# Kernel tuning notes

Hardware: AMD Instinct MI355X
Metric: run time of the kernel (lower is better)

## Reference

```python
import jax, jax.numpy as jnp
import numpy as np

HEADS = 4
TOKEN_CH = 128
D_HEAD = TOKEN_CH // HEADS  # 32


def setup_inputs() -> dict:
    key = jax.random.key(0)
    ks = jax.random.split(key, 12)
    B, QC, Z, H, W = 4, 256, 16, 32, 32
    N, KVC = 256, 512
    s = lambda k, shape, fan: jax.random.normal(k, shape, jnp.float32) * (1.0 / np.sqrt(fan))
    return {
        "feat":   jax.random.normal(ks[0], (B, QC, Z, H, W), jnp.float32),
        "tokens": jax.random.normal(ks[1], (B, N, KVC), jnp.float32),
        "qw":   s(ks[2], (TOKEN_CH, QC), QC),      # Conv3d 1x1 -> [out, in]
        "qb":   jnp.zeros((TOKEN_CH,), jnp.float32),
        "kw":   s(ks[3], (TOKEN_CH, KVC), KVC),    # Linear, no bias
        "vw":   s(ks[4], (TOKEN_CH, KVC), KVC),
        "projw": s(ks[5], (QC, TOKEN_CH), TOKEN_CH),
        "projb": jnp.zeros((QC,), jnp.float32),
        "ff1w": s(ks[6], (QC * 2, QC), QC),
        "ff1b": jnp.zeros((QC * 2,), jnp.float32),
        "ff2w": s(ks[7], (QC, QC * 2), QC * 2),
        "ff2b": jnp.zeros((QC,), jnp.float32),
        "gate": jnp.zeros((1,), jnp.float32),
    }


def _conv1x1(x, w, b):
    # x: [B, Cin, Z, H, W], w: [Cout, Cin] -> [B, Cout, Z, H, W]
    return jnp.einsum('bczhw,oc->bozhw', x, w) + b[None, :, None, None, None]


def reference(feat, tokens, qw, qb, kw, vw, projw, projb, ff1w, ff1b, ff2w, ff2b, gate):
    B, C, Z, H, W = feat.shape
    S = Z * H * W
    scale = D_HEAD ** (-0.5)

    # Q: conv1x1 then split heads -> [B, nh, S, dh]
    q = _conv1x1(feat, qw, qb).reshape(B, HEADS, D_HEAD, S).transpose(0, 1, 3, 2)
    # K, V: linear (no bias) -> [B, nh, N, dh]
    k = jnp.einsum('bnc,tc->bnt', tokens, kw).reshape(B, -1, HEADS, D_HEAD).transpose(0, 2, 1, 3)
    v = jnp.einsum('bnc,tc->bnt', tokens, vw).reshape(B, -1, HEADS, D_HEAD).transpose(0, 2, 1, 3)

    attn = jax.nn.softmax(jnp.einsum('bhsd,bhnd->bhsn', q, k) * scale, axis=-1)
    out = jnp.einsum('bhsn,bhnd->bhsd', attn, v)  # [B, nh, S, dh]

    # merge heads back to channel-first volume: b (nh dh) z h w
    out = out.transpose(0, 1, 3, 2).reshape(B, TOKEN_CH, Z, H, W)
    out = _conv1x1(out, projw, projb)

    out = feat + jnp.tanh(gate[0]) * out
    ff = _conv1x1(jax.nn.silu(_conv1x1(out, ff1w, ff1b)), ff2w, ff2b)
    return out + ff
```

## Files before the change

kernel.cpp:

```cpp
#include <hip/hip_runtime.h>

#define NB 4
#define QC 256
#define SD 16384
#define NT 256
#define KVC 512
#define TC 128
#define NH 4
#define DH 32
#define TSP 64

typedef unsigned short u16;
typedef unsigned int u32;
typedef __attribute__((ext_vector_type(8))) short bf16x8;
typedef __attribute__((ext_vector_type(4))) float f32x4;

__device__ __forceinline__ float b2f(u16 u) {
  unsigned int v = ((unsigned int)u) << 16;
  return __builtin_bit_cast(float, v);
}
__device__ __forceinline__ u16 f2b(float f) {
  unsigned int x = __builtin_bit_cast(unsigned int, f);
  unsigned int r = (x + 0x7fffu + ((x >> 16) & 1u)) >> 16;
  return (u16)r;
}
__device__ __forceinline__ u16 f2b_fast(float f) {
  return (u16)((__builtin_bit_cast(unsigned int, f) + 0x8000u) >> 16);
}
__device__ __forceinline__ u32 pk2(float a, float b) {
  u32 ua = __builtin_bit_cast(u32, a) + 0x8000u;
  u32 ub = __builtin_bit_cast(u32, b) + 0x8000u;
  return __builtin_amdgcn_perm(ub, ua, 0x07060302u);
}

__device__ __forceinline__ int swz(int row, int col) {
  return (row << 8) + (col ^ ((row & 7) << 3));
}

__global__ __launch_bounds__(256) void prep_kernel(
    const float* __restrict__ ff1w, const float* __restrict__ ff2w,
    u16* __restrict__ w1p, u16* __restrict__ w2p,
    const float* __restrict__ tokens, const float* __restrict__ kw,
    const float* __restrict__ vw, const float* __restrict__ gate,
    float* __restrict__ ws_kv) {
  int bid = blockIdx.x;
  if (bid < 128) {
    int idx = bid * 256 + threadIdx.x;
    int lane = idx & 63;
    int m = lane & 15, q = lane >> 4;
    if (idx < 16384) {
      int kblk = (idx >> 6) & 7;
      int jblk = idx >> 9;
      const float* src = ff1w + (size_t)(jblk * 16 + m) * QC + kblk * 32 + q * 8;
      u16* dst = w1p + (size_t)idx * 8;
#pragma unroll
      for (int i = 0; i < 8; i++) dst[i] = f2b(src[i]);
    } else {
      int s2 = idx - 16384;
      int kblk = (s2 >> 6) & 15;
      int oblk = s2 >> 10;
      const float* src = ff2w + (size_t)(oblk * 16 + m) * KVC + kblk * 32 + q * 8;
      u16* dst = w2p + (size_t)s2 * 8;
#pragma unroll
      for (int i = 0; i < 8; i++) dst[i] = f2b(src[i]);
    }
  }
  float tg = tanhf(gate[0]);
  if (tg == 0.0f) return;
  {
    int b = bid >> 8;
    int n = bid & 255;
    __shared__ float tok[KVC];
    for (int c = threadIdx.x; c < KVC; c += 256)
      tok[c] = tokens[((size_t)(b * NT + n)) * KVC + c];
    __syncthreads();
    int tid = threadIdx.x;
    int t = tid & 127;
    const float* w = (tid < 128) ? kw : vw;
    const float* wr = w + (size_t)t * KVC;
    float acc = 0.f;
    for (int c = 0; c < KVC; c += 4) {
      float4 wv = *(const float4*)(wr + c);
      acc += tok[c] * wv.x + tok[c + 1] * wv.y + tok[c + 2] * wv.z + tok[c + 3] * wv.w;
    }
    int h = t >> 5, d = t & 31;
    float* dst = ws_kv + ((tid < 128) ? 0 : NB * NH * NT * DH);
    dst[(((b * NH + h) * NT) + n) * DH + d] = acc;
  }
}

__global__ __launch_bounds__(512, 4) void fused_kernel(
    const float* __restrict__ feat, const float* __restrict__ qw,
    const float* __restrict__ qb, const float* __restrict__ projw,
    const float* __restrict__ projb, const float* __restrict__ ff1b,
    const float* __restrict__ ff2b, const u16* __restrict__ w1p,
    const u16* __restrict__ w2p, const float* __restrict__ gate,
    const float* __restrict__ ws_kv, float* __restrict__ out) {
  __shared__ u16 sX[64 * 256];
  __shared__ u16 sH[64 * 256];

  int b = blockIdx.x >> 8;
  int s0 = (blockIdx.x & 255) * TSP;
  int tid = threadIdx.x;
  int w = tid >> 6;
  int lane = tid & 63;
  int lm = lane & 15, lq = lane >> 4;

  {
    const float* fb = feat + (((size_t)b * QC) << 14) + s0;
    int cq = (tid >> 4) * 4;
    int sq = (tid & 15) * 4;
#pragma unroll
    for (int it = 0; it < 2; ++it) {
      int c = it * 128 + cq;
      float4 r0 = *(const float4*)(fb + ((size_t)(c + 0) << 14) + sq);
      float4 r1 = *(const float4*)(fb + ((size_t)(c + 1) << 14) + sq);
      float4 r2 = *(const float4*)(fb + ((size_t)(c + 2) << 14) + sq);
      float4 r3 = *(const float4*)(fb + ((size_t)(c + 3) << 14) + sq);
      uint2 d0, d1, d2, d3;
      d0.x = pk2(r0.x, r1.x); d0.y = pk2(r2.x, r3.x);
      d1.x = pk2(r0.y, r1.y); d1.y = pk2(r2.y, r3.y);
      d2.x = pk2(r0.z, r1.z); d2.y = pk2(r2.z, r3.z);
      d3.x = pk2(r0.w, r1.w); d3.y = pk2(r2.w, r3.w);
      *(uint2*)&sX[swz(sq + 0, c)] = d0;
      *(uint2*)&sX[swz(sq + 1, c)] = d1;
      *(uint2*)&sX[swz(sq + 2, c)] = d2;
      *(uint2*)&sX[swz(sq + 3, c)] = d3;
    }
  }
  float tg = tanhf(gate[0]);
  __syncthreads();

  if (tg != 0.0f) {
    if (w < 4) {
      float qreg[DH];
#pragma unroll
      for (int d = 0; d < DH; d++) {
        int o = w * DH + d;
        float a = qb[o];
        const float* qr = qw + (size_t)o * QC;
        for (int c = 0; c < QC; c += 4) {
          float4 wv = *(const float4*)(qr + c);
          a += b2f(sX[swz(lane, c + 0)]) * wv.x;
          a += b2f(sX[swz(lane, c + 1)]) * wv.y;
          a += b2f(sX[swz(lane, c + 2)]) * wv.z;
          a += b2f(sX[swz(lane, c + 3)]) * wv.w;
        }
        qreg[d] = a;
      }
      const float* Kp = ws_kv + (size_t)(b * NH + w) * NT * DH;
      const float* Vp = Kp + NB * NH * NT * DH;
      float m_ = -1e30f, l_ = 0.f;
      float oacc[DH];
#pragma unroll
      for (int d = 0; d < DH; d++) oacc[d] = 0.f;
      const float scale = 0.17677669529663687f;
      for (int n = 0; n < NT; n++) {
        const float* kr = Kp + n * DH;
        float s = 0.f;
#pragma unroll
        for (int d = 0; d < DH; d++) s += qreg[d] * kr[d];
        s *= scale;
        float nm = fmaxf(m_, s);
        float p = __expf(s - nm);
        float al = __expf(m_ - nm);
        const float* vr = Vp + n * DH;
        l_ = l_ * al + p;
#pragma unroll
        for (int d = 0; d < DH; d++) oacc[d] = oacc[d] * al + p * vr[d];
        m_ = nm;
      }
      float inv = 1.0f / l_;
#pragma unroll
      for (int d = 0; d < DH; d++)
        sH[swz(lane, w * DH + d)] = f2b(oacc[d] * inv);
    }
    __syncthreads();
    for (int ci = 0; ci < 32; ci++) {
      int c = w * 32 + ci;
      float a = projb[c];
      const float* pr = projw + (size_t)c * TC;
      for (int t = 0; t < TC; t += 4) {
        float4 wv = *(const float4*)(pr + t);
        a += b2f(sH[swz(lane, t + 0)]) * wv.x;
        a += b2f(sH[swz(lane, t + 1)]) * wv.y;
        a += b2f(sH[swz(lane, t + 2)]) * wv.z;
        a += b2f(sH[swz(lane, t + 3)]) * wv.w;
      }
      float o1 = b2f(sX[swz(lane, c)]) + tg * a;
      sX[swz(lane, c)] = f2b(o1);
    }
    __syncthreads();
  }

  f32x4 acc2[2][4];
#pragma unroll
  for (int t = 0; t < 2; t++) {
    float b2v = ff2b[(w * 2 + t) * 16 + lm];
    f32x4 iv = {b2v, b2v, b2v, b2v};
#pragma unroll
    for (int m = 0; m < 4; m++) acc2[t][m] = iv;
  }

#pragma unroll 1
  for (int ch = 0; ch < 2; ++ch) {
    f32x4 acc1[2][4];
#pragma unroll
    for (int t = 0; t < 2; t++) {
      float b1v = ff1b[ch * 256 + (w * 2 + t) * 16 + lm];
      f32x4 iv = {b1v, b1v, b1v, b1v};
#pragma unroll
      for (int m = 0; m < 4; m++) acc1[t][m] = iv;
    }
    {
      int jb0 = ch * 16 + w * 2;
      const u16* p0 = w1p + (((size_t)jb0 * 8) * 64 + lane) * 8;
      const u16* p1 = p0 + 4096;
      bf16x8 c0 = *(const bf16x8*)(p0);
      bf16x8 c1 = *(const bf16x8*)(p1);
      bf16x8 n0 = *(const bf16x8*)(p0 + 512);
      bf16x8 n1 = *(const bf16x8*)(p1 + 512);
#pragma unroll
      for (int k = 0; k < 8; ++k) {
        bf16x8 f0, f1;
        if (k < 6) {
          f0 = *(const bf16x8*)(p0 + (size_t)(k + 2) * 512);
          f1 = *(const bf16x8*)(p1 + (size_t)(k + 2) * 512);
        }
        int col = k * 32 + lq * 8;
#pragma unroll
        for (int m = 0; m < 4; m++) {
          bf16x8 a = *(const bf16x8*)&sX[swz(m * 16 + lm, col)];
          acc1[0][m] = __builtin_amdgcn_mfma_f32_16x16x32_bf16(a, c0, acc1[0][m], 0, 0, 0);
          acc1[1][m] = __builtin_amdgcn_mfma_f32_16x16x32_bf16(a, c1, acc1[1][m], 0, 0, 0);
        }
        c0 = n0; c1 = n1;
        if (k < 6) { n0 = f0; n1 = f1; }
      }
    }
    __syncthreads();
#pragma unroll
    for (int t = 0; t < 2; t++) {
      int jl = (w * 2 + t) * 16 + lm;
#pragma unroll
      for (int m = 0; m < 4; m++) {
        int sb = m * 16 + lq * 4;
        f32x4 v = acc1[t][m];
#pragma unroll
        for (int r = 0; r < 4; r++) {
          float x = v[r];
          float sl = x * __builtin_amdgcn_rcpf(1.f + __expf(-x));
          sH[swz(sb + r, jl)] = f2b_fast(sl);
        }
      }
    }
    const u16* qp0 = w2p + (((size_t)((w * 2) * 16 + ch * 8)) * 64 + lane) * 8;
    const u16* qp1 = qp0 + 8192;
    bf16x8 d0 = *(const bf16x8*)(qp0);
    bf16x8 d1 = *(const bf16x8*)(qp1);
    bf16x8 e0 = *(const bf16x8*)(qp0 + 512);
    bf16x8 e1 = *(const bf16x8*)(qp1 + 512);
    __syncthreads();
#pragma unroll
    for (int k = 0; k < 8; ++k) {
      bf16x8 f0, f1;
      if (k < 6) {
        f0 = *(const bf16x8*)(qp0 + (size_t)(k + 2) * 512);
        f1 = *(const bf16x8*)(qp1 + (size_t)(k + 2) * 512);
      }
      int col = k * 32 + lq * 8;
#pragma unroll
      for (int m = 0; m < 4; m++) {
        bf16x8 a = *(const bf16x8*)&sH[swz(m * 16 + lm, col)];
        acc2[0][m] = __builtin_amdgcn_mfma_f32_16x16x32_bf16(a, d0, acc2[0][m], 0, 0, 0);
        acc2[1][m] = __builtin_amdgcn_mfma_f32_16x16x32_bf16(a, d1, acc2[1][m], 0, 0, 0);
      }
      d0 = e0; d1 = e1;
      if (k < 6) { e0 = f0; e1 = f1; }
    }
  }

#pragma unroll
  for (int t = 0; t < 2; t++) {
    int c = (w * 2 + t) * 16 + lm;
#pragma unroll
    for (int m = 0; m < 4; m++) {
      int sb = m * 16 + lq * 4;
      f32x4 v = acc2[t][m];
      float4 ov;
      ov.x = v[0] + b2f(sX[swz(sb + 0, c)]);
      ov.y = v[1] + b2f(sX[swz(sb + 1, c)]);
      ov.z = v[2] + b2f(sX[swz(sb + 2, c)]);
      ov.w = v[3] + b2f(sX[swz(sb + 3, c)]);
      *(float4*)(out + (((size_t)(b * QC + c)) << 14) + s0 + sb) = ov;
    }
  }
}

extern "C" void kernel_launch(void* const* d_in, const int* in_sizes, int n_in,
                              void* d_out, int out_size, void* d_ws, size_t ws_size,
                              hipStream_t stream) {
  const float* feat   = (const float*)d_in[0];
  const float* tokens = (const float*)d_in[1];
  const float* qw     = (const float*)d_in[2];
  const float* qb     = (const float*)d_in[3];
  const float* kw     = (const float*)d_in[4];
  const float* vw     = (const float*)d_in[5];
  const float* projw  = (const float*)d_in[6];
  const float* projb  = (const float*)d_in[7];
  const float* ff1w   = (const float*)d_in[8];
  const float* ff1b   = (const float*)d_in[9];
  const float* ff2w   = (const float*)d_in[10];
  const float* ff2b   = (const float*)d_in[11];
  const float* gate   = (const float*)d_in[12];
  float* out = (float*)d_out;

  u16* w1p = (u16*)d_ws;
  u16* w2p = w1p + 131072;
  float* ws_kv = (float*)((char*)d_ws + 524288);

  prep_kernel<<<dim3(NB * NT), dim3(256), 0, stream>>>(
      ff1w, ff2w, w1p, w2p, tokens, kw, vw, gate, ws_kv);
  fused_kernel<<<dim3(NB * (SD / TSP)), dim3(512), 0, stream>>>(
      feat, qw, qb, projw, projb, ff1b, ff2b, w1p, w2p, gate, ws_kv, out);
}
```

Before: 208.7 us.

## Split FFN hidden into four chunks with double-buffered LDS to drop a barrier

The FFN hidden dimension is now processed in four chunks of 128 instead of two chunks of 256. The hidden staging buffer is split into two halves that alternate per chunk. This lets the barrier before the SiLU write be removed, since consecutive chunks write to different buffers, and it halves the per-chunk accumulator registers. In exchange there are more loop iterations with shorter MFMA chains, and correctness depends on one barrier per chunk being enough to separate reuse of the same buffer two chunks apart.

New measurement: 171.4 us. 1.22x faster.

```diff
diff --git a/kernel.cpp b/kernel.cpp
--- a/kernel.cpp
+++ b/kernel.cpp
@@ -35,6 +35,9 @@
 
 __device__ __forceinline__ int swz(int row, int col) {
   return (row << 8) + (col ^ ((row & 7) << 3));
+}
+__device__ __forceinline__ int swzH(int row, int col) {
+  return (row << 7) + (col ^ ((row & 7) << 3));
 }
 
 __global__ __launch_bounds__(256) void prep_kernel(
@@ -97,7 +100,7 @@
     const u16* __restrict__ w2p, const float* __restrict__ gate,
     const float* __restrict__ ws_kv, float* __restrict__ out) {
   __shared__ u16 sX[64 * 256];
-  __shared__ u16 sH[64 * 256];
+  __shared__ u16 sH[2][64 * 128];
 
   int b = blockIdx.x >> 8;
   int s0 = (blockIdx.x & 255) * TSP;
@@ -173,7 +176,7 @@
       float inv = 1.0f / l_;
 #pragma unroll
       for (int d = 0; d < DH; d++)
-        sH[swz(lane, w * DH + d)] = f2b(oacc[d] * inv);
+        sH[0][swzH(lane, w * DH + d)] = f2b(oacc[d] * inv);
     }
     __syncthreads();
     for (int ci = 0; ci < 32; ci++) {
@@ -182,10 +185,10 @@
       const float* pr = projw + (size_t)c * TC;
       for (int t = 0; t < TC; t += 4) {
         float4 wv = *(const float4*)(pr + t);
-        a += b2f(sH[swz(lane, t + 0)]) * wv.x;
-        a += b2f(sH[swz(lane, t + 1)]) * wv.y;
-        a += b2f(sH[swz(lane, t + 2)]) * wv.z;
-        a += b2f(sH[swz(lane, t + 3)]) * wv.w;
+        a += b2f(sH[0][swzH(lane, t + 0)]) * wv.x;
+        a += b2f(sH[0][swzH(lane, t + 1)]) * wv.y;
+        a += b2f(sH[0][swzH(lane, t + 2)]) * wv.z;
+        a += b2f(sH[0][swzH(lane, t + 3)]) * wv.w;
       }
       float o1 = b2f(sX[swz(lane, c)]) + tg * a;
       sX[swz(lane, c)] = f2b(o1);
@@ -203,58 +206,48 @@
   }
 
 #pragma unroll 1
-  for (int ch = 0; ch < 2; ++ch) {
-    f32x4 acc1[2][4];
-#pragma unroll
-    for (int t = 0; t < 2; t++) {
-      float b1v = ff1b[ch * 256 + (w * 2 + t) * 16 + lm];
+  for (int ch = 0; ch < 4; ++ch) {
+    u16* sHh = sH[ch & 1];
+    f32x4 acc1[4];
+    {
+      float b1v = ff1b[(ch * 8 + w) * 16 + lm];
       f32x4 iv = {b1v, b1v, b1v, b1v};
 #pragma unroll
-      for (int m = 0; m < 4; m++) acc1[t][m] = iv;
+      for (int m = 0; m < 4; m++) acc1[m] = iv;
     }
     {
-      int jb0 = ch * 16 + w * 2;
-      const u16* p0 = w1p + (((size_t)jb0 * 8) * 64 + lane) * 8;
-      const u16* p1 = p0 + 4096;
+      const u16* p0 = w1p + (((size_t)(ch * 8 + w) * 8) * 64 + lane) * 8;
       bf16x8 c0 = *(const bf16x8*)(p0);
-      bf16x8 c1 = *(const bf16x8*)(p1);
       bf16x8 n0 = *(const bf16x8*)(p0 + 512);
-      bf16x8 n1 = *(const bf16x8*)(p1 + 512);
 #pragma unroll
       for (int k = 0; k < 8; ++k) {
-        bf16x8 f0, f1;
-        if (k < 6) {
-          f0 = *(const bf16x8*)(p0 + (size_t)(k + 2) * 512);
-          f1 = *(const bf16x8*)(p1 + (size_t)(k + 2) * 512);
-        }
+        bf16x8 f0;
+        if (k < 6) f0 = *(const bf16x8*)(p0 + (size_t)(k + 2) * 512);
         int col = k * 32 + lq * 8;
 #pragma unroll
         for (int m = 0; m < 4; m++) {
           bf16x8 a = *(const bf16x8*)&sX[swz(m * 16 + lm, col)];
-          acc1[0][m] = __builtin_amdgcn_mfma_f32_16x16x32_bf16(a, c0, acc1[0][m], 0, 0, 0);
-          acc1[1][m] = __builtin_amdgcn_mfma_f32_16x16x32_bf16(a, c1, acc1[1][m], 0, 0, 0);
+          acc1[m] = __builtin_amdgcn_mfma_f32_16x16x32_bf16(a, c0, acc1[m], 0, 0, 0);
         }
-        c0 = n0; c1 = n1;
-        if (k < 6) { n0 = f0; n1 = f1; }
-      }
-    }
-    __syncthreads();
-#pragma unroll
-    for (int t = 0; t < 2; t++) {
-      int jl = (w * 2 + t) * 16 + lm;
+        c0 = n0;
+        if (k < 6) n0 = f0;
+      }
+    }
+    {
+      int jl = w * 16 + lm;
 #pragma unroll
       for (int m = 0; m < 4; m++) {
         int sb = m * 16 + lq * 4;
-        f32x4 v = acc1[t][m];
+        f32x4 v = acc1[m];
 #pragma unroll
         for (int r = 0; r < 4; r++) {
           float x = v[r];
           float sl = x * __builtin_amdgcn_rcpf(1.f + __expf(-x));
-          sH[swz(sb + r, jl)] = f2b_fast(sl);
+          sHh[swzH(sb + r, jl)] = f2b_fast(sl);
         }
       }
     }
-    const u16* qp0 = w2p + (((size_t)((w * 2) * 16 + ch * 8)) * 64 + lane) * 8;
+    const u16* qp0 = w2p + (((size_t)((w * 2) * 16 + ch * 4)) * 64 + lane) * 8;
     const u16* qp1 = qp0 + 8192;
     bf16x8 d0 = *(const bf16x8*)(qp0);
     bf16x8 d1 = *(const bf16x8*)(qp1);
@@ -262,21 +255,21 @@
     bf16x8 e1 = *(const bf16x8*)(qp1 + 512);
     __syncthreads();
 #pragma unroll
-    for (int k = 0; k < 8; ++k) {
+    for (int k = 0; k < 4; ++k) {
       bf16x8 f0, f1;
-      if (k < 6) {
+      if (k < 2) {
         f0 = *(const bf16x8*)(qp0 + (size_t)(k + 2) * 512);
         f1 = *(const bf16x8*)(qp1 + (size_t)(k + 2) * 512);
       }
       int col = k * 32 + lq * 8;
 #pragma unroll
       for (int m = 0; m < 4; m++) {
-        bf16x8 a = *(const bf16x8*)&sH[swz(m * 16 + lm, col)];
+        bf16x8 a = *(const bf16x8*)&sHh[swzH(m * 16 + lm, col)];
         acc2[0][m] = __builtin_amdgcn_mfma_f32_16x16x32_bf16(a, d0, acc2[0][m], 0, 0, 0);
         acc2[1][m] = __builtin_amdgcn_mfma_f32_16x16x32_bf16(a, d1, acc2[1][m], 0, 0, 0);
       }
       d0 = e0; d1 = e1;
-      if (k < 6) { e0 = f0; e1 = f1; }
+      if (k < 2) { e0 = f0; e1 = f1; }
     }
   }
 
```
